# Kernel optimization log

Measured on AMD Instinct MI355X. Metric: run time of the kernel, lower is better.

Reference implementation:

```python
import jax, jax.numpy as jnp
import numpy as np

B, K, N, F = 32, 4, 512, 128


def setup_inputs() -> dict:
    key = jax.random.key(0)
    k1, k2, k3, k4 = jax.random.split(key, 4)
    H = jax.random.normal(k1, (B, N, F), dtype=jnp.float32)
    E = jax.random.uniform(k2, (B, K, N, N), dtype=jnp.float32)
    # xavier_normal_ equivalents
    rw_std = float(np.sqrt(2.0 / (F + F * K)))  # torch xavier treats last dims
    RW = jax.random.normal(k3, (F, F, K), dtype=jnp.float32) * rw_std
    sw_std = float(np.sqrt(2.0 / (F + F)))
    SW = jax.random.normal(k4, (F, F), dtype=jnp.float32) * sw_std
    return {"H": H, "E": E, "RW": RW, "SW": SW}


def reference(H, E, RW, SW):
    # D = 1 / sum over (k, i) of (E + I)  -> [b, n]
    n = E.shape[2]
    D = 1.0 / (E + jnp.eye(n, dtype=E.dtype)).sum(axis=(1, 2))  # [b, n]
    # relational aggregation: sum_{k,j,m} E[b,k,i,j] H[b,j,m] RW[m,f,k] -> [b,i,f]
    rel = jnp.einsum('bkij,bjm,mfk->bif', E, H, RW)
    self_term = jnp.einsum('bjf,fl->bjl', H, SW)
    return jax.nn.sigmoid(D[:, :, None] * rel + self_term)
```

## Files before the change

kernel.cpp:

```cpp
#include <hip/hip_runtime.h>
#include <hip/hip_bf16.h>

#define B_ 32
#define K_ 4
#define N_ 512
#define F_ 128

typedef __attribute__((ext_vector_type(8))) short short8;
typedef __attribute__((ext_vector_type(4))) float float4v;

__device__ __forceinline__ unsigned short f2bf(float x) {
    unsigned int u = __builtin_bit_cast(unsigned int, x);
    u += 0x7FFFu + ((u >> 16) & 1u);
    return (unsigned short)(u >> 16);
}

__device__ __forceinline__ short8 pack8(float4v a, float4v b) {
    short8 r;
    r[0] = (short)f2bf(a[0]); r[1] = (short)f2bf(a[1]);
    r[2] = (short)f2bf(a[2]); r[3] = (short)f2bf(a[3]);
    r[4] = (short)f2bf(b[0]); r[5] = (short)f2bf(b[1]);
    r[6] = (short)f2bf(b[2]); r[7] = (short)f2bf(b[3]);
    return r;
}

__global__ void k0_weights(const float* __restrict__ RW, const float* __restrict__ SW,
                           unsigned short* __restrict__ Wt, unsigned short* __restrict__ SWt) {
    int r = blockIdx.x;
    int m = threadIdx.x;
    if (r < 512) {
        int k = r >> 7, f = r & 127;
        Wt[r * F_ + m] = f2bf(RW[(m * F_ + f) * K_ + k]);
    } else {
        int l = r - 512;
        SWt[l * F_ + m] = f2bf(SW[m * F_ + l]);
    }
}

__global__ void k1_colsum(const float* __restrict__ E, float* __restrict__ colsum) {
    int bid = blockIdx.x;
    int b   = bid >> 5;
    int jt  = (bid >> 4) & 1;
    int isl = bid & 15;
    int j   = jt * 256 + threadIdx.x;
    int i0  = isl * 32;
    float s0 = 0.f, s1 = 0.f, s2 = 0.f, s3 = 0.f;
#pragma unroll
    for (int k = 0; k < K_; ++k) {
        const float* p = E + ((size_t)((b * K_ + k) * N_ + i0)) * N_ + j;
#pragma unroll 4
        for (int ii = 0; ii < 32; ii += 4) {
            s0 += p[(ii + 0) * N_];
            s1 += p[(ii + 1) * N_];
            s2 += p[(ii + 2) * N_];
            s3 += p[(ii + 3) * N_];
        }
    }
    atomicAdd(&colsum[b * N_ + j], (s0 + s1) + (s2 + s3));
}

__global__ void k2_expand(const float* __restrict__ H, const unsigned short* __restrict__ Wt,
                          unsigned short* __restrict__ Tt) {
    int bid = blockIdx.x;
    int b  = bid >> 5;
    int ct = (bid >> 2) & 7;
    int jt = bid & 3;
    int lane = threadIdx.x & 63;
    int wv   = threadIdx.x >> 6;
    int c0 = ct * 64 + wv * 16;
    int jbase = jt * 128;
    int lrow = lane & 15, lgrp = lane >> 4;

    float4v acc[8];
#pragma unroll
    for (int i = 0; i < 8; ++i) acc[i] = {0.f, 0.f, 0.f, 0.f};

#pragma unroll
    for (int ms = 0; ms < 4; ++ms) {
        int m0 = ms * 32;
        short8 a = *(const short8*)(Wt + (c0 + lrow) * F_ + m0 + lgrp * 8);
#pragma unroll
        for (int cf = 0; cf < 8; ++cf) {
            int j = jbase + cf * 16 + lrow;
            const float* hp = H + ((size_t)b * N_ + j) * F_ + m0 + lgrp * 8;
            float4v h0 = *(const float4v*)hp;
            float4v h1 = *(const float4v*)(hp + 4);
            short8 bb = pack8(h0, h1);
            acc[cf] = __builtin_amdgcn_mfma_f32_16x16x32_bf16(a, bb, acc[cf], 0, 0, 0);
        }
    }
#pragma unroll
    for (int cf = 0; cf < 8; ++cf) {
#pragma unroll
        for (int r = 0; r < 4; ++r) {
            int c = c0 + lgrp * 4 + r;
            int j = jbase + cf * 16 + lrow;
            Tt[((size_t)b * 512 + c) * N_ + j] = f2bf(acc[cf][r]);
        }
    }
}

__global__ void __launch_bounds__(512)
k3_fuse(const float* __restrict__ E, const float* __restrict__ H,
        const unsigned short* __restrict__ Tt, const unsigned short* __restrict__ SWt,
        const float* __restrict__ colsum, float* __restrict__ out) {
    int bid = blockIdx.x;
    int b  = bid >> 3;
    int it = bid & 7;
    int lane = threadIdx.x & 63;
    int wv   = threadIdx.x >> 6;
    int i0 = it * 64 + (wv >> 1) * 16;
    int f0 = (wv & 1) * 64;
    int lrow = lane & 15, lgrp = lane >> 4;

    float4v accR[4], accS[4];
#pragma unroll
    for (int i = 0; i < 4; ++i) { accR[i] = {0.f, 0.f, 0.f, 0.f}; accS[i] = {0.f, 0.f, 0.f, 0.f}; }

    for (int k = 0; k < K_; ++k) {
        const float* Eb = E + ((size_t)((b * K_ + k) * N_ + i0 + lrow)) * N_;
        const unsigned short* Tb = Tt + ((size_t)b * 512 + k * 128 + f0) * N_;
#pragma unroll 2
        for (int js = 0; js < 16; ++js) {
            int j0 = js * 32;
            const float* ep = Eb + j0 + lgrp * 8;
            float4v e0 = *(const float4v*)ep;
            float4v e1 = *(const float4v*)(ep + 4);
            short8 a = pack8(e0, e1);
#pragma unroll
            for (int cf = 0; cf < 4; ++cf) {
                const unsigned short* tp = Tb + (size_t)(cf * 16 + lrow) * N_ + j0 + lgrp * 8;
                short8 bb = *(const short8*)tp;
                accR[cf] = __builtin_amdgcn_mfma_f32_16x16x32_bf16(a, bb, accR[cf], 0, 0, 0);
            }
        }
    }

    {
        const float* Hp = H + ((size_t)b * N_ + i0 + lrow) * F_;
#pragma unroll
        for (int ms = 0; ms < 4; ++ms) {
            int m0 = ms * 32;
            const float* hp = Hp + m0 + lgrp * 8;
            float4v h0 = *(const float4v*)hp;
            float4v h1 = *(const float4v*)(hp + 4);
            short8 a = pack8(h0, h1);
#pragma unroll
            for (int cf = 0; cf < 4; ++cf) {
                const unsigned short* sp = SWt + (f0 + cf * 16 + lrow) * F_ + m0 + lgrp * 8;
                short8 bb = *(const short8*)sp;
                accS[cf] = __builtin_amdgcn_mfma_f32_16x16x32_bf16(a, bb, accS[cf], 0, 0, 0);
            }
        }
    }

    float Dv[4];
#pragma unroll
    for (int r = 0; r < 4; ++r) {
        int i = i0 + lgrp * 4 + r;
        Dv[r] = 1.0f / (colsum[b * N_ + i] + (float)K_);
    }
#pragma unroll
    for (int cf = 0; cf < 4; ++cf) {
#pragma unroll
        for (int r = 0; r < 4; ++r) {
            int i = i0 + lgrp * 4 + r;
            int f = f0 + cf * 16 + lrow;
            float x = Dv[r] * accR[cf][r] + accS[cf][r];
            out[((size_t)b * N_ + i) * F_ + f] = 1.0f / (1.0f + __expf(-x));
        }
    }
}

extern "C" void kernel_launch(void* const* d_in, const int* in_sizes, int n_in,
                              void* d_out, int out_size, void* d_ws, size_t ws_size,
                              hipStream_t stream) {
    const float* H  = (const float*)d_in[0];
    const float* E  = (const float*)d_in[1];
    const float* RW = (const float*)d_in[2];
    const float* SW = (const float*)d_in[3];
    float* out = (float*)d_out;

    char* ws = (char*)d_ws;
    unsigned short* Wt  = (unsigned short*)(ws);
    unsigned short* SWt = (unsigned short*)(ws + 131072);
    float* colsum       = (float*)(ws + 163840);
    unsigned short* Tt  = (unsigned short*)(ws + 262144);

    hipMemsetAsync(colsum, 0, B_ * N_ * sizeof(float), stream);
    k0_weights<<<640, 128, 0, stream>>>(RW, SW, Wt, SWt);
    k1_colsum<<<1024, 256, 0, stream>>>(E, colsum);
    k2_expand<<<1024, 256, 0, stream>>>(H, Wt, Tt);
    k3_fuse<<<256, 512, 0, stream>>>(E, H, Tt, SWt, colsum, out);
}
```

Before: 329.0 us.

## Pre-convert E to bf16 during column-sum pass and split relational GEMM over j

The colsum pass now also writes a bf16 copy of E, so the main relational GEMM reads half the bytes and skips per-tile conversion. The relational GEMM is split into two j-halves, doubling the block count, and is software-pipelined with double-buffered register loads. Partial results go to an fp32 workspace and are combined in a separate epilogue kernel that also computes the self term and the sigmoid. This adds an extra write and read of E in bf16, plus the partial-sum traffic, and falls back to the old path when the workspace is too small.

```diff
diff --git a/kernel.cpp b/kernel.cpp
--- a/kernel.cpp
+++ b/kernel.cpp
@@ -7,6 +7,7 @@
 #define F_ 128
 
 typedef __attribute__((ext_vector_type(8))) short short8;
+typedef __attribute__((ext_vector_type(4))) short short4v;
 typedef __attribute__((ext_vector_type(4))) float float4v;
 
 __device__ __forceinline__ unsigned short f2bf(float x) {
@@ -37,6 +38,188 @@
     }
 }
 
+__global__ void k1v2_convert(const float* __restrict__ E, float* __restrict__ colsum,
+                             unsigned short* __restrict__ Ebf) {
+    int bid = blockIdx.x;
+    int b   = bid >> 5;
+    int isl = (bid >> 1) & 15;
+    int jt  = bid & 1;
+    int t   = threadIdx.x;
+    int j   = jt * 256 + (t & 63) * 4;
+    int r0  = isl * 32 + (t >> 6) * 8;
+
+    float cs0 = 0.f, cs1 = 0.f, cs2 = 0.f, cs3 = 0.f;
+#pragma unroll
+    for (int k = 0; k < K_; ++k) {
+        const float* Ep = E + ((size_t)((b * K_ + k) * N_ + r0)) * N_ + j;
+        unsigned short* Op = Ebf + ((size_t)((b * K_ + k) * N_ + r0)) * N_ + j;
+#pragma unroll
+        for (int r = 0; r < 8; ++r) {
+            float4v v = *(const float4v*)(Ep + (size_t)r * N_);
+            cs0 += v[0]; cs1 += v[1]; cs2 += v[2]; cs3 += v[3];
+            short4v s;
+            s[0] = (short)f2bf(v[0]); s[1] = (short)f2bf(v[1]);
+            s[2] = (short)f2bf(v[2]); s[3] = (short)f2bf(v[3]);
+            *(short4v*)(Op + (size_t)r * N_) = s;
+        }
+    }
+    atomicAdd(&colsum[b * N_ + j + 0], cs0);
+    atomicAdd(&colsum[b * N_ + j + 1], cs1);
+    atomicAdd(&colsum[b * N_ + j + 2], cs2);
+    atomicAdd(&colsum[b * N_ + j + 3], cs3);
+}
+
+__global__ void k2_expand(const float* __restrict__ H, const unsigned short* __restrict__ Wt,
+                          unsigned short* __restrict__ Tt) {
+    int bid = blockIdx.x;
+    int b  = bid >> 5;
+    int ct = (bid >> 2) & 7;
+    int jt = bid & 3;
+    int lane = threadIdx.x & 63;
+    int wv   = threadIdx.x >> 6;
+    int c0 = ct * 64 + wv * 16;
+    int jbase = jt * 128;
+    int lrow = lane & 15, lgrp = lane >> 4;
+
+    float4v acc[8];
+#pragma unroll
+    for (int i = 0; i < 8; ++i) acc[i] = {0.f, 0.f, 0.f, 0.f};
+
+#pragma unroll
+    for (int ms = 0; ms < 4; ++ms) {
+        int m0 = ms * 32;
+        short8 a = *(const short8*)(Wt + (c0 + lrow) * F_ + m0 + lgrp * 8);
+#pragma unroll
+        for (int cf = 0; cf < 8; ++cf) {
+            int j = jbase + cf * 16 + lrow;
+            const float* hp = H + ((size_t)b * N_ + j) * F_ + m0 + lgrp * 8;
+            float4v h0 = *(const float4v*)hp;
+            float4v h1 = *(const float4v*)(hp + 4);
+            short8 bb = pack8(h0, h1);
+            acc[cf] = __builtin_amdgcn_mfma_f32_16x16x32_bf16(a, bb, acc[cf], 0, 0, 0);
+        }
+    }
+#pragma unroll
+    for (int cf = 0; cf < 8; ++cf) {
+#pragma unroll
+        for (int r = 0; r < 4; ++r) {
+            int c = c0 + lgrp * 4 + r;
+            int j = jbase + cf * 16 + lrow;
+            Tt[((size_t)b * 512 + c) * N_ + j] = f2bf(acc[cf][r]);
+        }
+    }
+}
+
+__global__ void __launch_bounds__(512)
+k3v2_rel(const unsigned short* __restrict__ Ebf, const unsigned short* __restrict__ Tt,
+         float* __restrict__ relP) {
+    int bid = blockIdx.x;
+    int b  = bid >> 4;
+    int it = (bid >> 1) & 7;
+    int jc = bid & 1;
+    int lane = threadIdx.x & 63;
+    int wv   = threadIdx.x >> 6;
+    int i0 = it * 64 + (wv >> 1) * 16;
+    int f0 = (wv & 1) * 64;
+    int lrow = lane & 15, lgrp = lane >> 4;
+    int jbase = jc * 256;
+
+    float4v acc[4];
+#pragma unroll
+    for (int i = 0; i < 4; ++i) acc[i] = {0.f, 0.f, 0.f, 0.f};
+
+    const unsigned short* Eb = Ebf + ((size_t)(b * K_) * N_ + (i0 + lrow)) * N_ + jbase + lgrp * 8;
+    const unsigned short* Tb = Tt + ((size_t)b * 512 + f0 + lrow) * N_ + jbase + lgrp * 8;
+
+#define EA(t) (const short8*)(Eb + ((t) >> 3) * 262144 + ((t) & 7) * 32)
+#define TA(t, cf) (const short8*)(Tb + ((t) >> 3) * 65536 + (cf) * 8192 + ((t) & 7) * 32)
+
+    short8 a0, b00, b01, b02, b03;
+    short8 a1, b10, b11, b12, b13;
+    a0 = *EA(0); b00 = *TA(0, 0); b01 = *TA(0, 1); b02 = *TA(0, 2); b03 = *TA(0, 3);
+
+    for (int t = 0; t < 32; t += 2) {
+        int t1 = t + 1;
+        int t2 = (t + 2 < 32) ? t + 2 : 31;
+        a1 = *EA(t1); b10 = *TA(t1, 0); b11 = *TA(t1, 1); b12 = *TA(t1, 2); b13 = *TA(t1, 3);
+        acc[0] = __builtin_amdgcn_mfma_f32_16x16x32_bf16(a0, b00, acc[0], 0, 0, 0);
+        acc[1] = __builtin_amdgcn_mfma_f32_16x16x32_bf16(a0, b01, acc[1], 0, 0, 0);
+        acc[2] = __builtin_amdgcn_mfma_f32_16x16x32_bf16(a0, b02, acc[2], 0, 0, 0);
+        acc[3] = __builtin_amdgcn_mfma_f32_16x16x32_bf16(a0, b03, acc[3], 0, 0, 0);
+        a0 = *EA(t2); b00 = *TA(t2, 0); b01 = *TA(t2, 1); b02 = *TA(t2, 2); b03 = *TA(t2, 3);
+        acc[0] = __builtin_amdgcn_mfma_f32_16x16x32_bf16(a1, b10, acc[0], 0, 0, 0);
+        acc[1] = __builtin_amdgcn_mfma_f32_16x16x32_bf16(a1, b11, acc[1], 0, 0, 0);
+        acc[2] = __builtin_amdgcn_mfma_f32_16x16x32_bf16(a1, b12, acc[2], 0, 0, 0);
+        acc[3] = __builtin_amdgcn_mfma_f32_16x16x32_bf16(a1, b13, acc[3], 0, 0, 0);
+    }
+#undef EA
+#undef TA
+
+    float* dst = relP + (size_t)jc * (B_ * N_ * F_);
+#pragma unroll
+    for (int cf = 0; cf < 4; ++cf) {
+#pragma unroll
+        for (int r = 0; r < 4; ++r) {
+            int i = i0 + lgrp * 4 + r;
+            int f = f0 + cf * 16 + lrow;
+            dst[((size_t)b * N_ + i) * F_ + f] = acc[cf][r];
+        }
+    }
+}
+
+__global__ void __launch_bounds__(512)
+k4_epi(const float* __restrict__ relP, const float* __restrict__ H,
+       const unsigned short* __restrict__ SWt, const float* __restrict__ colsum,
+       float* __restrict__ out) {
+    int bid = blockIdx.x;
+    int b  = bid >> 3;
+    int it = bid & 7;
+    int lane = threadIdx.x & 63;
+    int wv   = threadIdx.x >> 6;
+    int i0 = it * 64 + (wv >> 1) * 16;
+    int f0 = (wv & 1) * 64;
+    int lrow = lane & 15, lgrp = lane >> 4;
+
+    float4v accS[4];
+#pragma unroll
+    for (int i = 0; i < 4; ++i) accS[i] = {0.f, 0.f, 0.f, 0.f};
+
+    const float* Hp = H + ((size_t)b * N_ + i0 + lrow) * F_;
+#pragma unroll
+    for (int ms = 0; ms < 4; ++ms) {
+        int m0 = ms * 32;
+        const float* hp = Hp + m0 + lgrp * 8;
+        float4v h0 = *(const float4v*)hp;
+        float4v h1 = *(const float4v*)(hp + 4);
+        short8 a = pack8(h0, h1);
+#pragma unroll
+        for (int cf = 0; cf < 4; ++cf) {
+            const unsigned short* sp = SWt + (f0 + cf * 16 + lrow) * F_ + m0 + lgrp * 8;
+            short8 bb = *(const short8*)sp;
+            accS[cf] = __builtin_amdgcn_mfma_f32_16x16x32_bf16(a, bb, accS[cf], 0, 0, 0);
+        }
+    }
+
+    float Dv[4];
+#pragma unroll
+    for (int r = 0; r < 4; ++r) {
+        int i = i0 + lgrp * 4 + r;
+        Dv[r] = 1.0f / (colsum[b * N_ + i] + (float)K_);
+    }
+#pragma unroll
+    for (int cf = 0; cf < 4; ++cf) {
+#pragma unroll
+        for (int r = 0; r < 4; ++r) {
+            int i = i0 + lgrp * 4 + r;
+            int f = f0 + cf * 16 + lrow;
+            size_t idx = ((size_t)b * N_ + i) * F_ + f;
+            float v = relP[idx] + relP[idx + (size_t)B_ * N_ * F_];
+            float x = Dv[r] * v + accS[cf][r];
+            out[idx] = 1.0f / (1.0f + __expf(-x));
+        }
+    }
+}
+
 __global__ void k1_colsum(const float* __restrict__ E, float* __restrict__ colsum) {
     int bid = blockIdx.x;
     int b   = bid >> 5;
@@ -57,47 +240,6 @@
         }
     }
     atomicAdd(&colsum[b * N_ + j], (s0 + s1) + (s2 + s3));
-}
-
-__global__ void k2_expand(const float* __restrict__ H, const unsigned short* __restrict__ Wt,
-                          unsigned short* __restrict__ Tt) {
-    int bid = blockIdx.x;
-    int b  = bid >> 5;
-    int ct = (bid >> 2) & 7;
-    int jt = bid & 3;
-    int lane = threadIdx.x & 63;
-    int wv   = threadIdx.x >> 6;
-    int c0 = ct * 64 + wv * 16;
-    int jbase = jt * 128;
-    int lrow = lane & 15, lgrp = lane >> 4;
-
-    float4v acc[8];
-#pragma unroll
-    for (int i = 0; i < 8; ++i) acc[i] = {0.f, 0.f, 0.f, 0.f};
-
-#pragma unroll
-    for (int ms = 0; ms < 4; ++ms) {
-        int m0 = ms * 32;
-        short8 a = *(const short8*)(Wt + (c0 + lrow) * F_ + m0 + lgrp * 8);
-#pragma unroll
-        for (int cf = 0; cf < 8; ++cf) {
-            int j = jbase + cf * 16 + lrow;
-            const float* hp = H + ((size_t)b * N_ + j) * F_ + m0 + lgrp * 8;
-            float4v h0 = *(const float4v*)hp;
-            float4v h1 = *(const float4v*)(hp + 4);
-            short8 bb = pack8(h0, h1);
-            acc[cf] = __builtin_amdgcn_mfma_f32_16x16x32_bf16(a, bb, acc[cf], 0, 0, 0);
-        }
-    }
-#pragma unroll
-    for (int cf = 0; cf < 8; ++cf) {
-#pragma unroll
-        for (int r = 0; r < 4; ++r) {
-            int c = c0 + lgrp * 4 + r;
-            int j = jbase + cf * 16 + lrow;
-            Tt[((size_t)b * 512 + c) * N_ + j] = f2bf(acc[cf][r]);
-        }
-    }
 }
 
 __global__ void __launch_bounds__(512)
@@ -135,7 +277,6 @@
             }
         }
     }
-
     {
         const float* Hp = H + ((size_t)b * N_ + i0 + lrow) * F_;
 #pragma unroll
@@ -153,7 +294,6 @@
             }
         }
     }
-
     float Dv[4];
 #pragma unroll
     for (int r = 0; r < 4; ++r) {
@@ -186,10 +326,21 @@
     unsigned short* SWt = (unsigned short*)(ws + 131072);
     float* colsum       = (float*)(ws + 163840);
     unsigned short* Tt  = (unsigned short*)(ws + 262144);
+    unsigned short* Ebf = (unsigned short*)(ws + 17039360);
+    float* relP         = (float*)(ws + 84148224);
+    const size_t WS_NEED = 100925440ull;
 
     hipMemsetAsync(colsum, 0, B_ * N_ * sizeof(float), stream);
     k0_weights<<<640, 128, 0, stream>>>(RW, SW, Wt, SWt);
-    k1_colsum<<<1024, 256, 0, stream>>>(E, colsum);
-    k2_expand<<<1024, 256, 0, stream>>>(H, Wt, Tt);
-    k3_fuse<<<256, 512, 0, stream>>>(E, H, Tt, SWt, colsum, out);
-}
+
+    if (ws_size >= WS_NEED) {
+        k1v2_convert<<<1024, 256, 0, stream>>>(E, colsum, Ebf);
+        k2_expand<<<1024, 256, 0, stream>>>(H, Wt, Tt);
+        k3v2_rel<<<512, 512, 0, stream>>>(Ebf, Tt, relP);
+        k4_epi<<<256, 512, 0, stream>>>(relP, H, SWt, colsum, out);
+    } else {
+        k1_colsum<<<1024, 256, 0, stream>>>(E, colsum);
+        k2_expand<<<1024, 256, 0, stream>>>(H, Wt, Tt);
+        k3_fuse<<<256, 512, 0, stream>>>(E, H, Tt, SWt, colsum, out);
+    }
+}
```

New measurement: 339.8 us. 1.03x slower.
